# Kernel tuning notes

Measured on AMD Instinct MI355X. Metric: run time of the kernel, lower is better.

Reference implementation:

```python
import jax, jax.numpy as jnp
import numpy as np


def _build_basic_label(size):
    # [size, size, 2] with entries (i, j)
    ii, jj = jnp.meshgrid(jnp.arange(size, dtype=jnp.float32),
                          jnp.arange(size, dtype=jnp.float32), indexing='ij')
    return jnp.stack([ii, jj], axis=-1)


def setup_inputs() -> dict:
    key = jax.random.key(0)
    x = jax.random.normal(key, (64, 512, 28, 28), dtype=jnp.float32)
    return {"x": x}


def reference(x):
    N, C, H, W = x.shape
    size = H
    HW = H * W

    # channel-sum saliency mask, per-sample mean threshold
    mask = jnp.sum(x, axis=1).reshape(N, HW)                 # [N, HW]
    thresholds = jnp.mean(mask, axis=1, keepdims=True)       # [N, 1]
    binary_mask = (mask > thresholds).astype(x.dtype)        # [N, HW]

    x_flat = x.reshape(N, C, HW)                             # [N, C, HW]
    masked_x = x_flat * binary_mask[:, None, :]              # [N, C, HW]
    # torch: masked_x -> [N, HW, C], mean over C, argmax over HW
    scores = jnp.mean(masked_x, axis=1)                      # [N, HW]
    reduced_x_max_index = jnp.argmax(scores, axis=1)         # [N]

    label = _build_basic_label(size).reshape(HW, 2)          # [HW, 2]
    basic_anchor = label[reduced_x_max_index]                # [N, 2]

    relative_coord = (label[None, :, :] - basic_anchor[:, None, :]) / size  # [N, HW, 2]
    relative_dist = jnp.sqrt(jnp.sum(relative_coord ** 2, axis=-1))          # [N, HW]
    relative_angle = jnp.arctan2(relative_coord[:, :, 1], relative_coord[:, :, 0])
    relative_angle = (relative_angle / np.pi + 1.0) / 2.0                    # [N, HW]

    relative_coord_total = jnp.stack([relative_dist, relative_angle], axis=-1)  # [N, HW, 2]

    # rank-1 outer product of channel-mean positional weight
    position_weight = jnp.mean(x_flat, axis=1)               # [N, HW]
    position_weight = position_weight[:, :, None] * position_weight[:, None, :]  # [N, HW, HW]

    return relative_coord_total, basic_anchor, position_weight
```

## Files before the change

### kernel.cpp

```cpp
#include <hip/hip_runtime.h>
#include <math.h>

#define NB   64
#define CCH  512
#define SZ   28
#define HW   784
#define NCHUNK 8
#define CPC  (CCH / NCHUNK)
#define Q4   (HW / 4)

#define OFF_ANCHOR 100352
#define OFF_PW     100480

__global__ __launch_bounds__(256) void k_partial(const float* __restrict__ x,
                                                 float* __restrict__ partial) {
    const int chunk = blockIdx.x;
    const int n     = blockIdx.y;
    const int t     = threadIdx.x;
    if (t >= Q4) return;

    const float* xp = x + (size_t)n * CCH * HW + (size_t)chunk * CPC * HW + 4 * t;
    float4 acc = make_float4(0.f, 0.f, 0.f, 0.f);
    #pragma unroll 4
    for (int c = 0; c < CPC; ++c) {
        float4 v = *(const float4*)(xp + (size_t)c * HW);
        acc.x += v.x; acc.y += v.y; acc.z += v.z; acc.w += v.w;
    }
    *(float4*)(partial + ((size_t)n * NCHUNK + chunk) * HW + 4 * t) = acc;
}

__global__ __launch_bounds__(256) void k_reduce(const float* __restrict__ partial,
                                                float* __restrict__ out,
                                                float* __restrict__ pw) {
    const int n = blockIdx.x;
    const int t = threadIdx.x;

    __shared__ float mask[HW];
    __shared__ float red[256];
    __shared__ int   redi[256];

    float local = 0.f;
    if (t < Q4) {
        float4 acc = make_float4(0.f, 0.f, 0.f, 0.f);
        #pragma unroll
        for (int ch = 0; ch < NCHUNK; ++ch) {
            float4 v = *(const float4*)(partial + ((size_t)n * NCHUNK + ch) * HW + 4 * t);
            acc.x += v.x; acc.y += v.y; acc.z += v.z; acc.w += v.w;
        }
        *(float4*)(mask + 4 * t) = acc;
        local = acc.x + acc.y + acc.z + acc.w;
    }

    red[t] = local;
    __syncthreads();
    for (int s = 128; s > 0; s >>= 1) {
        if (t < s) red[t] += red[t + s];
        __syncthreads();
    }
    const float thr = red[0] * (1.0f / HW);
    __syncthreads();

    float bv = -INFINITY; int bp = HW;
    for (int p = t; p < HW; p += 256) {
        float m = mask[p];
        float s = (m > thr) ? m * (1.0f / CCH) : 0.0f;
        if (s > bv) { bv = s; bp = p; }
    }
    red[t] = bv; redi[t] = bp;
    __syncthreads();
    for (int s = 128; s > 0; s >>= 1) {
        if (t < s) {
            float ov = red[t + s]; int op = redi[t + s];
            if (ov > red[t] || (ov == red[t] && op < redi[t])) { red[t] = ov; redi[t] = op; }
        }
        __syncthreads();
    }
    const int   idx = redi[0];
    const float ai  = (float)(idx / SZ);
    const float aj  = (float)(idx % SZ);

    if (t == 0) {
        out[OFF_ANCHOR + n * 2 + 0] = ai;
        out[OFF_ANCHOR + n * 2 + 1] = aj;
    }

    const float inv_sz = 1.0f / (float)SZ;
    const float inv_pi = 0.31830988618367444f;
    for (int p = t; p < HW; p += 256) {
        float ci = ((float)(p / SZ) - ai) * inv_sz;
        float cj = ((float)(p % SZ) - aj) * inv_sz;
        float dist = sqrtf(ci * ci + cj * cj);
        float ang  = (atan2f(cj, ci) * inv_pi + 1.0f) * 0.5f;
        ((float2*)out)[(size_t)n * HW + p] = make_float2(dist, ang);
        pw[n * HW + p] = mask[p] * (1.0f / CCH);
    }
}

#define ROWS 8
__global__ __launch_bounds__(256) void k_outer(const float* __restrict__ pw,
                                               float* __restrict__ out) {
    const int tile = blockIdx.x;
    const int n    = blockIdx.y;
    const int t    = threadIdx.x;

    __shared__ float row[HW];
    if (t < Q4) ((float4*)row)[t] = ((const float4*)(pw + (size_t)n * HW))[t];
    __syncthreads();

    if (t >= Q4) return;
    float4 v = ((float4*)row)[t];
    float* obase = out + OFF_PW + ((size_t)n * HW + (size_t)tile * ROWS) * HW;
    #pragma unroll
    for (int r = 0; r < ROWS; ++r) {
        float a = row[tile * ROWS + r];
        float4 w = make_float4(a * v.x, a * v.y, a * v.z, a * v.w);
        ((float4*)(obase + (size_t)r * HW))[t] = w;
    }
}

extern "C" void kernel_launch(void* const* d_in, const int* in_sizes, int n_in,
                              void* d_out, int out_size, void* d_ws, size_t ws_size,
                              hipStream_t stream) {
    const float* x = (const float*)d_in[0];
    float* out = (float*)d_out;

    float* partial = (float*)d_ws;
    float* pw      = partial + (size_t)NB * NCHUNK * HW;

    k_partial<<<dim3(NCHUNK, NB), 256, 0, stream>>>(x, partial);
    k_reduce <<<dim3(NB),        256, 0, stream>>>(partial, out, pw);
    k_outer  <<<dim3(98, NB),    256, 0, stream>>>(pw, out);
}
```

Measured before the change: 48.78 us.

## Fuse channel reduce, argmax and outer-product kernels; use nontemporal loads and stores

Merges the per-sample reduce kernel and the outer-product kernel into one kernel with a 98x64 grid. Each block re-sums the 8 channel partials into shared memory and writes its 8 rows of the position-weight matrix. Only tile-0 blocks go on to compute the threshold, the argmax and the relative coordinates. This removes a kernel launch, the serialized 64-block reduce stage and the pw round trip through memory. In exchange, every block redundantly re-reads the partials from L2. The input loads and the large output writes now use nontemporal builtins to reduce cache pollution.

```diff
diff --git a/kernel.cpp b/kernel.cpp
--- a/kernel.cpp
+++ b/kernel.cpp
@@ -9,6 +9,8 @@
 #define CPC  (CCH / NCHUNK)
 #define Q4   (HW / 4)
 
+typedef float f4 __attribute__((ext_vector_type(4)));
+
 #define OFF_ANCHOR 100352
 #define OFF_PW     100480
 
@@ -19,37 +21,52 @@
     const int t     = threadIdx.x;
     if (t >= Q4) return;
 
-    const float* xp = x + (size_t)n * CCH * HW + (size_t)chunk * CPC * HW + 4 * t;
-    float4 acc = make_float4(0.f, 0.f, 0.f, 0.f);
+    const f4* xp = (const f4*)(x + (size_t)n * CCH * HW + (size_t)chunk * CPC * HW) + t;
+    f4 acc = (f4)(0.f);
     #pragma unroll 4
     for (int c = 0; c < CPC; ++c) {
-        float4 v = *(const float4*)(xp + (size_t)c * HW);
-        acc.x += v.x; acc.y += v.y; acc.z += v.z; acc.w += v.w;
+        f4 v = __builtin_nontemporal_load(xp + (size_t)c * Q4);
+        acc += v;
     }
-    *(float4*)(partial + ((size_t)n * NCHUNK + chunk) * HW + 4 * t) = acc;
+    *((f4*)(partial + ((size_t)n * NCHUNK + chunk) * HW) + t) = acc;
 }
 
-__global__ __launch_bounds__(256) void k_reduce(const float* __restrict__ partial,
-                                                float* __restrict__ out,
-                                                float* __restrict__ pw) {
-    const int n = blockIdx.x;
-    const int t = threadIdx.x;
+#define ROWS 8
+__global__ __launch_bounds__(256) void k_fused(const float* __restrict__ partial,
+                                               float* __restrict__ out) {
+    const int tile = blockIdx.x;
+    const int n    = blockIdx.y;
+    const int t    = threadIdx.x;
 
-    __shared__ float mask[HW];
+    __shared__ float row[HW];
     __shared__ float red[256];
     __shared__ int   redi[256];
 
     float local = 0.f;
     if (t < Q4) {
-        float4 acc = make_float4(0.f, 0.f, 0.f, 0.f);
+        f4 acc = (f4)(0.f);
         #pragma unroll
         for (int ch = 0; ch < NCHUNK; ++ch) {
-            float4 v = *(const float4*)(partial + ((size_t)n * NCHUNK + ch) * HW + 4 * t);
-            acc.x += v.x; acc.y += v.y; acc.z += v.z; acc.w += v.w;
+            acc += *((const f4*)(partial + ((size_t)n * NCHUNK + ch) * HW) + t);
         }
-        *(float4*)(mask + 4 * t) = acc;
+        acc *= (1.0f / (float)CCH);
+        ((f4*)row)[t] = acc;
         local = acc.x + acc.y + acc.z + acc.w;
     }
+    __syncthreads();
+
+    if (t < Q4) {
+        f4 v = ((f4*)row)[t];
+        float* obase = out + OFF_PW + ((size_t)n * HW + (size_t)tile * ROWS) * HW;
+        #pragma unroll
+        for (int r = 0; r < ROWS; ++r) {
+            float a = row[tile * ROWS + r];
+            f4 w = v * a;
+            __builtin_nontemporal_store(w, (f4*)(obase + (size_t)r * HW) + t);
+        }
+    }
+
+    if (tile != 0) return;
 
     red[t] = local;
     __syncthreads();
@@ -62,8 +79,8 @@
 
     float bv = -INFINITY; int bp = HW;
     for (int p = t; p < HW; p += 256) {
-        float m = mask[p];
-        float s = (m > thr) ? m * (1.0f / CCH) : 0.0f;
+        float m = row[p];
+        float s = (m > thr) ? m : 0.0f;
         if (s > bv) { bv = s; bp = p; }
     }
     red[t] = bv; redi[t] = bp;
@@ -92,29 +109,6 @@
         float dist = sqrtf(ci * ci + cj * cj);
         float ang  = (atan2f(cj, ci) * inv_pi + 1.0f) * 0.5f;
         ((float2*)out)[(size_t)n * HW + p] = make_float2(dist, ang);
-        pw[n * HW + p] = mask[p] * (1.0f / CCH);
-    }
-}
-
-#define ROWS 8
-__global__ __launch_bounds__(256) void k_outer(const float* __restrict__ pw,
-                                               float* __restrict__ out) {
-    const int tile = blockIdx.x;
-    const int n    = blockIdx.y;
-    const int t    = threadIdx.x;
-
-    __shared__ float row[HW];
-    if (t < Q4) ((float4*)row)[t] = ((const float4*)(pw + (size_t)n * HW))[t];
-    __syncthreads();
-
-    if (t >= Q4) return;
-    float4 v = ((float4*)row)[t];
-    float* obase = out + OFF_PW + ((size_t)n * HW + (size_t)tile * ROWS) * HW;
-    #pragma unroll
-    for (int r = 0; r < ROWS; ++r) {
-        float a = row[tile * ROWS + r];
-        float4 w = make_float4(a * v.x, a * v.y, a * v.z, a * v.w);
-        ((float4*)(obase + (size_t)r * HW))[t] = w;
     }
 }
 
@@ -125,9 +119,7 @@
     float* out = (float*)d_out;
 
     float* partial = (float*)d_ws;
-    float* pw      = partial + (size_t)NB * NCHUNK * HW;
 
     k_partial<<<dim3(NCHUNK, NB), 256, 0, stream>>>(x, partial);
-    k_reduce <<<dim3(NB),        256, 0, stream>>>(partial, out, pw);
-    k_outer  <<<dim3(98, NB),    256, 0, stream>>>(pw, out);
+    k_fused  <<<dim3(98, NB),     256, 0, stream>>>(partial, out);
 }
```

Result: slower. 50.70 us (+3.9%).
